# Kernel tuning notes

Hardware: AMD Instinct MI355X
Metric: run time of the kernel (lower is better)

The kernel has to match this reference:

```python
import jax, jax.numpy as jnp
import numpy as np

B, S, DIM = 4, 4096, 1024
H, DK, DV = 8, 64, 64
SEG = 512
EXP = 4
LN_EPS = 1e-5


def setup_inputs() -> dict:
    key = jax.random.key(0)
    ks = jax.random.split(key, 10)
    w = lambda i, shape: (jax.random.normal(ks[i], shape, jnp.float32) * 0.02)
    return {
        "x": jax.random.normal(ks[0], (B, S, DIM), jnp.float32),
        "Wq": w(1, (DIM, H * DK)),
        "Wk": w(2, (DIM, H * DK)),
        "Wv": w(3, (DIM, H * DV)),
        "Wo": w(4, (H * DV, DIM)),
        "betas": jax.random.normal(ks[5], (1, H, 1, DV), jnp.float32),
        "W1": w(6, (DIM, EXP * DIM)),
        "b1": jnp.zeros((EXP * DIM,), jnp.float32),
        "W2": w(7, (EXP * DIM, DIM)),
        "b2": jnp.zeros((DIM,), jnp.float32),
        "gamma": jnp.ones((DIM,), jnp.float32),
        "beta": jnp.zeros((DIM,), jnp.float32),
    }


def _compressive_memory(x, Wq, Wk, Wv, Wo, betas):
    b, s, _ = x.shape
    nseg = s // SEG
    # NOTE: original code does proj(x).unsqueeze(1).view(B, H, S, dk), i.e. a
    # pure reshape of (B, S*H*dk) -> (B, H, S, dk). We replicate it faithfully.
    qf = (x @ Wq).reshape(b, H, s, DK)
    kf = (x @ Wk).reshape(b, H, s, DK)
    vf = (x @ Wv).reshape(b, H, s, DV)
    # segment axis leading for scan: (nseg, B, H, SEG, d)
    seg_split = lambda t, d: t.reshape(b, H, nseg, SEG, d).transpose(2, 0, 1, 3, 4)
    qs, ks_, vs = seg_split(qf, DK), seg_split(kf, DK), seg_split(vf, DV)

    mem0 = jnp.zeros((b, H, DK, DV), jnp.float32)
    z0 = jnp.ones((b, H, DK, 1), jnp.float32) / DK
    causal_mask = jnp.tril(jnp.ones((SEG, SEG), bool))
    sig_b = jax.nn.sigmoid(betas)  # (1,H,1,DV)
    scale = 1.0 / (DK ** 0.5)

    def step(carry, seg):
        mem, z = carry
        q, k, v = seg  # (B,H,SEG,dk/dv)
        sigma_q = jax.nn.elu(q) + 1.0
        # memory retrieval
        att_mem = (sigma_q @ mem) / (sigma_q @ z)  # (B,H,SEG,DV)
        # local dot-product attention (causal)
        scores = jnp.einsum('bhik,bhjk->bhij', q, k) * scale
        scores = jnp.where(causal_mask, scores, -jnp.inf)
        att_dot = jax.nn.softmax(scores, axis=-1) @ v
        # linear memory update
        sigma_k = jax.nn.elu(k) + 1.0
        mem = mem + jnp.einsum('bhsk,bhsv->bhkv', sigma_k, v)
        z = z + sigma_k.sum(axis=-2, keepdims=True).transpose(0, 1, 3, 2)
        att = sig_b * att_mem + (1.0 - sig_b) * att_dot  # (B,H,SEG,DV)
        return (mem, z), att

    _, outs = jax.lax.scan(step, (mem0, z0), (qs, ks_, vs))
    # (nseg,B,H,SEG,DV) -> (B, nseg, SEG, H, DV) -> (B, S, H*DV)
    att = outs.transpose(1, 0, 3, 2, 4).reshape(b, s, H * DV)
    return att @ Wo


def reference(x, Wq, Wk, Wv, Wo, betas, W1, b1, W2, b2, gamma, beta):
    x_ = _compressive_memory(x, Wq, Wk, Wv, Wo, betas)
    # MLP: Linear -> ReLU -> Linear (dropout is identity at p=0.0)
    h = jax.nn.relu(x_ @ W1 + b1)
    x_ = h @ W2 + b2
    # residual + LayerNorm
    y = x_ + x
    mu = y.mean(axis=-1, keepdims=True)
    var = y.var(axis=-1, keepdims=True)
    return (y - mu) * jax.lax.rsqrt(var + LN_EPS) * gamma + beta
```

## Files before the change

kernel.cpp:

```cpp
#include <hip/hip_runtime.h>


typedef __attribute__((ext_vector_type(8))) short    short8;
typedef __attribute__((ext_vector_type(4))) float    f32x4;
typedef __attribute__((ext_vector_type(8))) unsigned short u16x8;
typedef __attribute__((ext_vector_type(4))) unsigned short u16x4;

#define B_    4
#define S_    4096
#define H_    8
#define SEG_  512
#define NSEG_ 8
#define QKVN  1536

__device__ __forceinline__ float bf2f(unsigned short u) {
  union { unsigned int i; float f; } x; x.i = ((unsigned int)u) << 16; return x.f;
}
__device__ __forceinline__ unsigned short f2bf(float f) {
  union { float f; unsigned int i; } x; x.f = f;
  unsigned int r = x.i + 0x7FFFu + ((x.i >> 16) & 1u);
  return (unsigned short)(r >> 16);
}
__device__ __forceinline__ float elu1(float x) { return x > 0.f ? x + 1.f : __expf(x); }

__device__ __forceinline__ void async_load16(const unsigned short* g, unsigned short* l) {
  __builtin_amdgcn_global_load_lds((const __attribute__((address_space(1))) void*)g,
                                   (__attribute__((address_space(3))) void*)l, 16, 0, 0);
}
__device__ __forceinline__ void wg_barrier() {
  asm volatile("" ::: "memory");
  __builtin_amdgcn_s_barrier();
  asm volatile("" ::: "memory");
}
__device__ __forceinline__ void vm_wait4() { asm volatile("s_waitcnt vmcnt(4)" ::: "memory"); }
__device__ __forceinline__ void vm_wait0() { asm volatile("s_waitcnt vmcnt(0)" ::: "memory"); }

__device__ __forceinline__ size_t qkv_addr(int b, int h, int seg, int i_seg, int d, int blk) {
  int r = h * 512 + seg * 64 + (i_seg >> 3);
  int c = ((i_seg & 7) << 6) + d;
  return ((size_t)b * S_ + r) * QKVN + blk + c;
}

__global__ void dtype_probe(const unsigned short* __restrict__ g, int* __restrict__ flag) {
  __shared__ int cnt;
  if (threadIdx.x == 0) cnt = 0;
  __syncthreads();
  int c = 0;
  for (int i = threadIdx.x; i < 1024; i += 256) c += (g[i] == 0x3F80u) ? 1 : 0;
  atomicAdd(&cnt, c);
  __syncthreads();
  if (threadIdx.x == 0) flag[0] = (cnt <= 768) ? 1 : 0;
}

__global__ void convert_small(const void* __restrict__ in, unsigned short* __restrict__ out,
                              int n, const int* __restrict__ flagp) {
  int i = blockIdx.x * 256 + threadIdx.x;
  if (i >= n) return;
  out[i] = (*flagp) ? f2bf(((const float*)in)[i]) : ((const unsigned short*)in)[i];
}

__global__ __launch_bounds__(256)
void convert_x(const void* __restrict__ in, unsigned short* __restrict__ out,
               int n8, const int* __restrict__ flagp) {
  int i = blockIdx.x * 256 + threadIdx.x;
  if (i >= n8) return;
  if (*flagp) {
    const f32x4* p = (const f32x4*)in;
    f32x4 a = p[(size_t)i * 2], b = p[(size_t)i * 2 + 1];
    u16x8 o;
    for (int j = 0; j < 4; j++) { o[j] = f2bf(a[j]); o[j + 4] = f2bf(b[j]); }
    *(u16x8*)(out + (size_t)i * 8) = o;
  } else {
    *(u16x8*)(out + (size_t)i * 8) = ((const u16x8*)in)[i];
  }
}

__global__ void transpose_any(const void* __restrict__ in, unsigned short* __restrict__ out,
                              int K, int N, const int* __restrict__ flagp) {
  __shared__ unsigned short tile[32][33];
  const int isf = *flagp;
  int n0 = blockIdx.x * 32, k0 = blockIdx.y * 32;
  int tx = threadIdx.x, ty = threadIdx.y;
  for (int j = 0; j < 4; j++) {
    size_t idx = (size_t)(k0 + ty + j * 8) * N + n0 + tx;
    tile[ty + j * 8][tx] = isf ? f2bf(((const float*)in)[idx]) : ((const unsigned short*)in)[idx];
  }
  __syncthreads();
  for (int j = 0; j < 4; j++)
    out[(size_t)(n0 + ty + j * 8) * K + k0 + tx] = tile[tx][ty + j * 8];
}

template <int HAS_BIAS, int RELU>
__global__ __launch_bounds__(512, 2)
void gemm256(const unsigned short* __restrict__ A,
             const unsigned short* __restrict__ Bt,
             const unsigned short* __restrict__ bias,
             unsigned short* __restrict__ C,
             int M, int N, int K) {
  __shared__ unsigned short smem[2][2][2][8192];
  const int tid = threadIdx.x;
  const int lane = tid & 63;
  const int w = tid >> 6;
  const int wr = w >> 2, wc = w & 3;
  const int l15 = lane & 15, quad = lane >> 4, l7 = lane & 7;

  const int nbx = N >> 8;
  const int nwg = (M >> 8) * nbx;
  const int orig = blockIdx.x;
  const int swz = (orig & 7) * (nwg >> 3) + (orig >> 3);
  const int m0 = (swz / nbx) << 8, n0 = (swz % nbx) << 8;

  const int srh = lane >> 3;
  const int sc = ((lane & 7) ^ srh) << 3;

  unsigned short* const A0p = &smem[0][0][0][0];
  unsigned short* const B0p = &smem[0][1][0][0];
  unsigned short* const A1p = &smem[1][0][0][0];
  unsigned short* const B1p = &smem[1][1][0][0];

  auto stA = [&](unsigned short* dst, int h, int kt) {
#pragma unroll
    for (int i2 = 0; i2 < 2; i2++) {
      const int seg = (i2 << 3) + w;
      const int r = (seg << 3) + srh;
      const int g = ((r >> 6) << 7) + (h << 6) + (r & 63);
      async_load16(A + (size_t)(m0 + g) * K + (kt << 6) + sc,
                   dst + (h << 13) + (seg << 9));
    }
  };
  auto stB = [&](unsigned short* dst, int h, int kt) {
#pragma unroll
    for (int i2 = 0; i2 < 2; i2++) {
      const int seg = (i2 << 3) + w;
      const int r = (seg << 3) + srh;
      const int g = ((r >> 5) << 6) + (h << 5) + (r & 31);
      async_load16(Bt + (size_t)(n0 + g) * K + (kt << 6) + sc,
                   dst + (h << 13) + (seg << 9));
    }
  };

  f32x4 acc[2][2][4][2] = {};
  short8 af[4][2], bfr[2][2];
  const int arow = (wr << 6) + l15;
  const int brow = (wc << 5) + l15;
  const int c0 = (quad ^ l7) << 3;
  const int c1 = ((4 + quad) ^ l7) << 3;

#define RD_A(BASE, MH) \
  { _Pragma("unroll") for (int mi = 0; mi < 4; mi++) { \
      const unsigned short* p_ = (BASE) + ((MH) << 13) + ((arow + mi * 16) << 6); \
      af[mi][0] = *(const short8*)(p_ + c0); \
      af[mi][1] = *(const short8*)(p_ + c1); } }
#define RD_B(BASE, NH) \
  { _Pragma("unroll") for (int ni = 0; ni < 2; ni++) { \
      const unsigned short* p_ = (BASE) + ((NH) << 13) + ((brow + ni * 16) << 6); \
      bfr[ni][0] = *(const short8*)(p_ + c0); \
      bfr[ni][1] = *(const short8*)(p_ + c1); } }
#define MFMA_Q(MH, NH) \
  { __builtin_amdgcn_s_setprio(1); \
    _Pragma("unroll") for (int mi = 0; mi < 4; mi++) \
    _Pragma("unroll") for (int ni = 0; ni < 2; ni++) { \
      acc[MH][NH][mi][ni] = __builtin_amdgcn_mfma_f32_16x16x32_bf16(af[mi][0], bfr[ni][0], acc[MH][NH][mi][ni], 0, 0, 0); \
      acc[MH][NH][mi][ni] = __builtin_amdgcn_mfma_f32_16x16x32_bf16(af[mi][1], bfr[ni][1], acc[MH][NH][mi][ni], 0, 0, 0); } \
    __builtin_amdgcn_s_setprio(0); }

  stA(A0p, 0, 0); stB(B0p, 1, 0); stA(A0p, 1, 0); stB(B0p, 0, 0);
  stA(A1p, 0, 1); stB(B1p, 1, 1);
  vm_wait4();
  wg_barrier();

  const int NI = K >> 7;
  for (int i = 0; i < NI; i++) {
    const int kt = i << 1;
    const bool nx = (i + 1 < NI);
    RD_A(A0p, 0) RD_B(B0p, 0)
    stA(A1p, 1, kt + 1);
    wg_barrier(); MFMA_Q(0, 0) wg_barrier();
    RD_B(B0p, 1)
    stB(B1p, 0, kt + 1);
    wg_barrier(); MFMA_Q(0, 1) wg_barrier();
    RD_A(A0p, 1)
    if (nx) stA(A0p, 0, kt + 2);
    wg_barrier(); MFMA_Q(1, 1) wg_barrier();
    RD_B(B0p, 0)
    if (nx) stB(B0p, 1, kt + 2);
    wg_barrier(); MFMA_Q(1, 0)
    if (nx) vm_wait4(); else vm_wait0();
    wg_barrier();
    RD_A(A1p, 0) RD_B(B1p, 0)
    if (nx) stA(A0p, 1, kt + 2);
    wg_barrier(); MFMA_Q(0, 0) wg_barrier();
    RD_B(B1p, 1)
    if (nx) stB(B0p, 0, kt + 2);
    wg_barrier(); MFMA_Q(0, 1) wg_barrier();
    RD_A(A1p, 1)
    if (nx) stA(A1p, 0, kt + 3);
    wg_barrier(); MFMA_Q(1, 1) wg_barrier();
    RD_B(B1p, 0)
    if (nx) stB(B1p, 1, kt + 3);
    wg_barrier(); MFMA_Q(1, 0)
    if (nx) vm_wait4(); else vm_wait0();
    wg_barrier();
  }
#undef RD_A
#undef RD_B
#undef MFMA_Q

#pragma unroll
  for (int mh = 0; mh < 2; mh++)
#pragma unroll
    for (int nh = 0; nh < 2; nh++)
#pragma unroll
      for (int ni = 0; ni < 2; ni++) {
        const int col = n0 + (wc << 6) + (nh << 5) + (ni << 4) + l15;
        const float bv = HAS_BIAS ? bf2f(bias[col]) : 0.f;
#pragma unroll
        for (int mi = 0; mi < 4; mi++) {
          const int rowb = m0 + (wr << 7) + (mh << 6) + (mi << 4) + (quad << 2);
#pragma unroll
          for (int r = 0; r < 4; r++) {
            float v = acc[mh][nh][mi][ni][r] + bv;
            if (RELU) v = v > 0.f ? v : 0.f;
            C[(size_t)(rowb + r) * N + col] = f2bf(v);
          }
        }
      }
}

template <int HAS_BIAS, int RELU, int RAWA>
__global__ __launch_bounds__(256, 4)
void gemm_bt(const void* __restrict__ A, size_t aoff,
             const unsigned short* __restrict__ Bt,
             const unsigned short* __restrict__ bias,
             unsigned short* __restrict__ C, int M, int N, int K,
             const int* __restrict__ flagp) {
  __shared__ unsigned short la[128 * 32];
  __shared__ unsigned short lb[128 * 32];
  const int isf = RAWA ? flagp[0] : 0;
  const int tid  = threadIdx.x;
  const int lane = tid & 63;
  const int w    = tid >> 6;
  const int wr   = w >> 1, wc = w & 1;
  const int m0 = blockIdx.y * 128, n0 = blockIdx.x * 128;
  const int l15 = lane & 15, quad = lane >> 4;
  const int lr = lane >> 2, l4 = lane & 3;
  f32x4 acc[4][4] = {};

  const int r0 = tid >> 2, kc0 = (tid & 3) * 8;
  const int r1 = r0 + 64;

  for (int k0 = 0; k0 < K; k0 += 32) {
    u16x8 a0v, a1v;
    if (RAWA && isf) {
      const float* Af = (const float*)A;
      size_t ia0 = aoff + (size_t)(m0 + r0) * K + k0 + kc0;
      size_t ia1 = aoff + (size_t)(m0 + r1) * K + k0 + kc0;
      f32x4 p0 = *(const f32x4*)(Af + ia0), p1 = *(const f32x4*)(Af + ia0 + 4);
      f32x4 p2 = *(const f32x4*)(Af + ia1), p3 = *(const f32x4*)(Af + ia1 + 4);
      for (int j = 0; j < 4; j++) {
        a0v[j] = f2bf(p0[j]); a0v[j + 4] = f2bf(p1[j]);
        a1v[j] = f2bf(p2[j]); a1v[j + 4] = f2bf(p3[j]);
      }
    }
    __syncthreads();
    if (!(RAWA && isf)) {
      const unsigned short* Au = (const unsigned short*)A + aoff;
      for (int i = 0; i < 2; i++) {
        int row = w * 32 + i * 16 + lr;
        async_load16(Au + (size_t)(m0 + row) * K + k0 + l4 * 8, la + (w * 32 + i * 16) * 32);
      }
    }
    for (int i = 0; i < 2; i++) {
      int row = w * 32 + i * 16 + lr;
      async_load16(Bt + (size_t)(n0 + row) * K + k0 + l4 * 8, lb + (w * 32 + i * 16) * 32);
    }
    if (RAWA && isf) {
      *(u16x8*)(la + r0 * 32 + kc0) = a0v;
      *(u16x8*)(la + r1 * 32 + kc0) = a1v;
    }
    __builtin_amdgcn_s_waitcnt(0x0F70);
    __syncthreads();
    short8 fa[4], fb[4];
    for (int mi = 0; mi < 4; mi++)
      fa[mi] = *(const short8*)(la + (wr * 64 + mi * 16 + l15) * 32 + quad * 8);
    for (int ni = 0; ni < 4; ni++)
      fb[ni] = *(const short8*)(lb + (wc * 64 + ni * 16 + l15) * 32 + quad * 8);
    for (int mi = 0; mi < 4; mi++)
      for (int ni = 0; ni < 4; ni++)
        acc[mi][ni] = __builtin_amdgcn_mfma_f32_16x16x32_bf16(fa[mi], fb[ni], acc[mi][ni], 0, 0, 0);
  }
  for (int ni = 0; ni < 4; ni++) {
    int col = n0 + wc * 64 + ni * 16 + l15;
    float bv = HAS_BIAS ? bf2f(bias[col]) : 0.f;
    for (int mi = 0; mi < 4; mi++) {
      int rowb = m0 + wr * 64 + mi * 16 + quad * 4;
      for (int r = 0; r < 4; r++) {
        float v = acc[mi][ni][r] + bv;
        if (RELU) v = v > 0.f ? v : 0.f;
        C[(size_t)(rowb + r) * N + col] = f2bf(v);
      }
    }
  }
}

__global__ __launch_bounds__(256)
void attn_stats(const unsigned short* __restrict__ qkv,
                float* __restrict__ Mseg, float* __restrict__ zseg) {
  int seg = blockIdx.x, h = blockIdx.y, b = blockIdx.z;
  __shared__ float sk[64][64];
  __shared__ float sv[64][64];
  int tid = threadIdx.x;
  int kidx = tid >> 2, vg = tid & 3;
  float acc[16] = {};
  float zacc = 0.f;
  for (int c = 0; c < 8; c++) {
    __syncthreads();
    for (int q = 0; q < 2; q++) {
      int cid = tid + q * 256;
      int row = cid >> 3, col = (cid & 7) * 8;
      int i_seg = c * 64 + row;
      u16x8 kv = *(const u16x8*)(qkv + qkv_addr(b, h, seg, i_seg, col, 512));
      u16x8 vv = *(const u16x8*)(qkv + qkv_addr(b, h, seg, i_seg, col, 1024));
      for (int j = 0; j < 8; j++) {
        sk[row][col + j] = elu1(bf2f(kv[j]));
        sv[row][col + j] = bf2f(vv[j]);
      }
    }
    __syncthreads();
    for (int i2 = 0; i2 < 64; i2++) {
      float s = sk[i2][kidx];
      if (vg == 0) zacc += s;
      for (int j = 0; j < 16; j++)
        acc[j] += s * sv[i2][vg * 16 + j];
    }
  }
  size_t ob = ((size_t)b * H_ + h) * NSEG_ + seg;
  float* mp = Mseg + ob * 4096;
  for (int j = 0; j < 16; j++)
    mp[kidx * 64 + vg * 16 + j] = acc[j];
  if (vg == 0) zseg[ob * 64 + kidx] = zacc;
}

__global__ __launch_bounds__(256)
void attn_prefix(float* __restrict__ Mseg, float* __restrict__ zseg) {
  int bh = blockIdx.x, tid = threadIdx.x;
  size_t mb = (size_t)bh * NSEG_ * 4096;
  for (int j = 0; j < 16; j++) {
    int e = tid + j * 256;
    float run = 0.f;
    for (int s = 0; s < NSEG_; s++) {
      float t = Mseg[mb + (size_t)s * 4096 + e];
      Mseg[mb + (size_t)s * 4096 + e] = run;
      run += t;
    }
  }
  if (tid < 64) {
    size_t zb = (size_t)bh * NSEG_ * 64;
    float run = 1.0f / 64.0f;
    for (int s = 0; s < NSEG_; s++) {
      float t = zseg[zb + (size_t)s * 64 + tid];
      zseg[zb + (size_t)s * 64 + tid] = run;
      run += t;
    }
  }
}

__global__ __launch_bounds__(256, 2)
void attn_core(const unsigned short* __restrict__ qkv, const unsigned short* __restrict__ betas_bf,
               const float* __restrict__ Mpre, const float* __restrict__ zpre,
               unsigned short* __restrict__ att) {
  const int t = blockIdx.x, seg = blockIdx.y;
  const int h = blockIdx.z & 7, b = blockIdx.z >> 3;
  __shared__ unsigned short q_lds[64 * 72];
  __shared__ unsigned short sq_lds[64 * 72];
  __shared__ unsigned short k_lds[64 * 72];
  __shared__ unsigned short vt_lds[64 * 72];
  __shared__ unsigned short p_lds[64 * 72];
  __shared__ unsigned short mt_lds[64 * 72];
  __shared__ float z_lds[64];
  __shared__ float den_lds[64];
  const int tid = threadIdx.x, lane = tid & 63, w = tid >> 6;
  const int l15 = lane & 15, quad = lane >> 4;
  size_t sbi = ((size_t)b * H_ + h) * NSEG_ + seg;
  const float* mp = Mpre + sbi * 4096;
  const float* zp = zpre + sbi * 64;

  for (int c = 0; c < 2; c++) {
    int idx = tid + c * 256;
    int row = idx >> 3, d0 = (idx & 7) * 8;
    u16x8 qv = *(const u16x8*)(qkv + qkv_addr(b, h, seg, t * 64 + row, d0, 0));
    u16x8 sv;
    for (int j = 0; j < 8; j++) sv[j] = f2bf(elu1(bf2f(qv[j])));
    *(u16x8*)(q_lds + row * 72 + d0) = qv;
    *(u16x8*)(sq_lds + row * 72 + d0) = sv;
    f32x4 m0 = *(const f32x4*)(mp + row * 64 + d0);
    f32x4 m1 = *(const f32x4*)(mp + row * 64 + d0 + 4);
    for (int j = 0; j < 4; j++) {
      mt_lds[(d0 + j) * 72 + row] = f2bf(m0[j]);
      mt_lds[(d0 + 4 + j) * 72 + row] = f2bf(m1[j]);
    }
  }
  if (tid < 64) z_lds[tid] = zp[tid];
  __syncthreads();
  if (tid < 64) {
    float d = 0.f;
    for (int k = 0; k < 64; k++) d += bf2f(sq_lds[tid * 72 + k]) * z_lds[k];
    den_lds[tid] = d;
  }
  f32x4 macc[4] = {};
  short8 qa0, qa1;
  {
    short8 a0 = *(const short8*)(sq_lds + (w * 16 + l15) * 72 + quad * 8);
    short8 a1 = *(const short8*)(sq_lds + (w * 16 + l15) * 72 + 32 + quad * 8);
    for (int nt = 0; nt < 4; nt++) {
      short8 b0 = *(const short8*)(mt_lds + (nt * 16 + l15) * 72 + quad * 8);
      short8 b1 = *(const short8*)(mt_lds + (nt * 16 + l15) * 72 + 32 + quad * 8);
      macc[nt] = __builtin_amdgcn_mfma_f32_16x16x32_bf16(a0, b0, macc[nt], 0, 0, 0);
      macc[nt] = __builtin_amdgcn_mfma_f32_16x16x32_bf16(a1, b1, macc[nt], 0, 0, 0);
    }
    qa0 = *(const short8*)(q_lds + (w * 16 + l15) * 72 + quad * 8);
    qa1 = *(const short8*)(q_lds + (w * 16 + l15) * 72 + 32 + quad * 8);
  }

  f32x4 oacc[4] = {};
  float lsum[4] = {0.f, 0.f, 0.f, 0.f};
  for (int kt = 0; kt <= t; kt++) {
    __syncthreads();
    for (int c = 0; c < 2; c++) {
      int idx = tid + c * 256;
      int row = idx >> 3, d0 = (idx & 7) * 8;
      u16x8 kv = *(const u16x8*)(qkv + qkv_addr(b, h, seg, kt * 64 + row, d0, 512));
      *(u16x8*)(k_lds + row * 72 + d0) = kv;
      u16x8 vv = *(const u16x8*)(qkv + qkv_addr(b, h, seg, kt * 64 + row, d0, 1024));
      for (int j = 0; j < 8; j++) vt_lds[(d0 + j) * 72 + row] = vv[j];
    }
    __syncthreads();
    float prow[4][4];
    for (int nt = 0; nt < 4; nt++) {
      short8 kb0 = *(const short8*)(k_lds + (nt * 16 + l15) * 72 + quad * 8);
      short8 kb1 = *(const short8*)(k_lds + (nt * 16 + l15) * 72 + 32 + quad * 8);
      f32x4 s = {};
      s = __builtin_amdgcn_mfma_f32_16x16x32_bf16(qa0, kb0, s, 0, 0, 0);
      s = __builtin_amdgcn_mfma_f32_16x16x32_bf16(qa1, kb1, s, 0, 0, 0);
      int jseg = kt * 64 + nt * 16 + l15;
      for (int r = 0; r < 4; r++) {
        int iseg = t * 64 + w * 16 + quad * 4 + r;
        prow[nt][r] = (jseg <= iseg) ? __expf(s[r] * 0.125f) : 0.f;
      }
    }
    for (int r = 0; r < 4; r++) {
      float rp = prow[0][r] + prow[1][r] + prow[2][r] + prow[3][r];
      rp += __shfl_xor(rp, 1); rp += __shfl_xor(rp, 2);
      rp += __shfl_xor(rp, 4); rp += __shfl_xor(rp, 8);
      lsum[r] += rp;
    }
    for (int nt = 0; nt < 4; nt++)
      for (int r = 0; r < 4; r++)
        p_lds[(w * 16 + quad * 4 + r) * 72 + nt * 16 + l15] = f2bf(prow[nt][r]);
    __syncthreads();
    short8 pa0 = *(const short8*)(p_lds + (w * 16 + l15) * 72 + quad * 8);
    short8 pa1 = *(const short8*)(p_lds + (w * 16 + l15) * 72 + 32 + quad * 8);
    for (int nt = 0; nt < 4; nt++) {
      short8 vb0 = *(const short8*)(vt_lds + (nt * 16 + l15) * 72 + quad * 8);
      short8 vb1 = *(const short8*)(vt_lds + (nt * 16 + l15) * 72 + 32 + quad * 8);
      oacc[nt] = __builtin_amdgcn_mfma_f32_16x16x32_bf16(pa0, vb0, oacc[nt], 0, 0, 0);
      oacc[nt] = __builtin_amdgcn_mfma_f32_16x16x32_bf16(pa1, vb1, oacc[nt], 0, 0, 0);
    }
  }
  __syncthreads();
  for (int nt = 0; nt < 4; nt++) {
    int v = nt * 16 + l15;
    float sb = 1.f / (1.f + __expf(-bf2f(betas_bf[h * 64 + v])));
    for (int r = 0; r < 4; r++) {
      int irow = w * 16 + quad * 4 + r;
      float am = macc[nt][r] / den_lds[irow];
      float ad = oacc[nt][r] / lsum[r];
      float o = sb * am + (1.f - sb) * ad;
      size_t orow = (size_t)b * S_ + (size_t)seg * SEG_ + t * 64 + irow;
      att[orow * 512 + h * 64 + v] = f2bf(o);
    }
  }
}

__global__ __launch_bounds__(256)
void ln_kernel(const unsigned short* __restrict__ x2, const void* __restrict__ xraw,
               const unsigned short* __restrict__ gamma_bf, const unsigned short* __restrict__ beta_bf,
               void* __restrict__ out, const int* __restrict__ flagp) {
  const int isf = *flagp;
  int row = blockIdx.x, tid = threadIdx.x;
  size_t rb = (size_t)row * 1024;
  u16x4 a = *(const u16x4*)(x2 + rb + tid * 4);
  float xv[4];
  if (isf) {
    f32x4 tv = *(const f32x4*)((const float*)xraw + rb + tid * 4);
    for (int j = 0; j < 4; j++) xv[j] = tv[j];
  } else {
    u16x4 tv = *(const u16x4*)((const unsigned short*)xraw + rb + tid * 4);
    for (int j = 0; j < 4; j++) xv[j] = bf2f(tv[j]);
  }
  float vv[4], s = 0.f, ss = 0.f;
  for (int j = 0; j < 4; j++) {
    vv[j] = bf2f(a[j]) + xv[j];
    s += vv[j]; ss += vv[j] * vv[j];
  }
  for (int off = 32; off >= 1; off >>= 1) { s += __shfl_xor(s, off); ss += __shfl_xor(ss, off); }
  __shared__ float ps[4], pss[4];
  int w = tid >> 6, lane = tid & 63;
  if (lane == 0) { ps[w] = s; pss[w] = ss; }
  __syncthreads();
  if (tid == 0) {
    float S = 0.f, SS = 0.f;
    for (int k = 0; k < 4; k++) { S += ps[k]; SS += pss[k]; }
    ps[0] = S; pss[0] = SS;
  }
  __syncthreads();
  float mean = ps[0] * (1.f / 1024.f);
  float var = pss[0] * (1.f / 1024.f) - mean * mean;
  float rs = rsqrtf(var + 1e-5f);
  u16x4 g = *(const u16x4*)(gamma_bf + tid * 4);
  u16x4 be = *(const u16x4*)(beta_bf + tid * 4);
  if (isf) {
    f32x4 o;
    for (int j = 0; j < 4; j++) o[j] = (vv[j] - mean) * rs * bf2f(g[j]) + bf2f(be[j]);
    *(f32x4*)((float*)out + rb + tid * 4) = o;
  } else {
    u16x4 o;
    for (int j = 0; j < 4; j++) o[j] = f2bf((vv[j] - mean) * rs * bf2f(g[j]) + bf2f(be[j]));
    *(u16x4*)((unsigned short*)out + rb + tid * 4) = o;
  }
}

extern "C" void kernel_launch(void* const* d_in, const int* in_sizes, int n_in,
                              void* d_out, int out_size, void* d_ws, size_t ws_size,
                              hipStream_t stream) {
  const void* x     = d_in[0];
  const void* Wq    = d_in[1];
  const void* Wk    = d_in[2];
  const void* Wv    = d_in[3];
  const void* Wo    = d_in[4];
  const void* betas = d_in[5];
  const void* W1    = d_in[6];
  const void* b1    = d_in[7];
  const void* W2    = d_in[8];
  const void* b2    = d_in[9];
  const void* gamma = d_in[10];
  const void* beta  = d_in[11];

  char* ws = (char*)d_ws;
  size_t off = 0;
  auto alloc = [&](size_t bytes) { char* p = ws + off; off += (bytes + 255) & ~(size_t)255; return p; };

  const int M = B_ * S_;
  int* flag = (int*)alloc(256);
  unsigned short* W1T = (unsigned short*)alloc((size_t)4096 * 1024 * 2);
  unsigned short* W2T = (unsigned short*)alloc((size_t)1024 * 4096 * 2);
  unsigned short* WqkvT = (unsigned short*)alloc((size_t)QKVN * 1024 * 2);
  unsigned short* WoT = (unsigned short*)alloc((size_t)1024 * 512 * 2);
  unsigned short* betas_bf = (unsigned short*)alloc(512 * 2);
  unsigned short* b1_bf    = (unsigned short*)alloc(4096 * 2);
  unsigned short* b2_bf    = (unsigned short*)alloc(1024 * 2);
  unsigned short* gamma_bf = (unsigned short*)alloc(1024 * 2);
  unsigned short* beta_bf  = (unsigned short*)alloc(1024 * 2);
  float* Mseg = (float*)alloc((size_t)B_ * H_ * NSEG_ * 4096 * 4);
  float* zseg = (float*)alloc((size_t)B_ * H_ * NSEG_ * 64 * 4);
  unsigned short* qkvb = (unsigned short*)alloc((size_t)M * QKVN * 2);
  unsigned short* x1   = qkvb;
  unsigned short* xbf  = (unsigned short*)d_out;
  unsigned short* attb = (unsigned short*)d_out;
  unsigned short* hbuf = (unsigned short*)d_out;

  if (off > ws_size) return;

  dtype_probe<<<1, 256, 0, stream>>>((const unsigned short*)gamma, flag);
  convert_small<<<2, 256, 0, stream>>>(betas, betas_bf, 512, flag);
  convert_small<<<16, 256, 0, stream>>>(b1, b1_bf, 4096, flag);
  convert_small<<<4, 256, 0, stream>>>(b2, b2_bf, 1024, flag);
  convert_small<<<4, 256, 0, stream>>>(gamma, gamma_bf, 1024, flag);
  convert_small<<<4, 256, 0, stream>>>(beta, beta_bf, 1024, flag);

  dim3 tb(32, 8);
  transpose_any<<<dim3(16, 32), tb, 0, stream>>>(Wq, WqkvT, 1024, 512, flag);
  transpose_any<<<dim3(16, 32), tb, 0, stream>>>(Wk, WqkvT + (size_t)512 * 1024, 1024, 512, flag);
  transpose_any<<<dim3(16, 32), tb, 0, stream>>>(Wv, WqkvT + (size_t)1024 * 1024, 1024, 512, flag);
  transpose_any<<<dim3(32, 16), tb, 0, stream>>>(Wo, WoT, 512, 1024, flag);
  transpose_any<<<dim3(128, 32), tb, 0, stream>>>(W1, W1T, 1024, 4096, flag);
  transpose_any<<<dim3(32, 128), tb, 0, stream>>>(W2, W2T, 4096, 1024, flag);

  convert_x<<<dim3((M * 1024 / 8 + 255) / 256), 256, 0, stream>>>(x, xbf, M * 1024 / 8, flag);

  gemm256<0, 0><<<dim3(384), 512, 0, stream>>>(xbf, WqkvT, nullptr, qkvb, M, QKVN, 1024);

  attn_stats<<<dim3(NSEG_, H_, B_), 256, 0, stream>>>(qkvb, Mseg, zseg);
  attn_prefix<<<dim3(B_ * H_), 256, 0, stream>>>(Mseg, zseg);
  attn_core<<<dim3(8, NSEG_, H_ * B_), 256, 0, stream>>>(qkvb, betas_bf, Mseg, zseg, attb);

  gemm256<0, 0><<<dim3(256), 512, 0, stream>>>(attb, WoT, nullptr, x1, M, 1024, 512);

  for (int c = 0; c < 2; c++) {
    unsigned short* x1c = x1 + (size_t)c * 8192 * 1024;
    gemm256<1, 1><<<dim3(512), 512, 0, stream>>>(x1c, W1T, b1_bf, hbuf, 8192, 4096, 1024);
    gemm_bt<1, 0, 0><<<dim3(8, 64), 256, 0, stream>>>(hbuf, 0, W2T, b2_bf, x1c, 8192, 1024, 4096, flag);
  }

  ln_kernel<<<dim3(M), 256, 0, stream>>>(x1, x, gamma_bf, beta_bf, d_out, flag);
}
```

Before: 776.3 us.

## Run MLP as whole-batch GEMMs with 256-tile kernel for W2 projection

The second MLP GEMM now uses the larger 256x256-tile gemm256 kernel instead of the 128-tile gemm_bt kernel, which is removed. When the workspace can hold the full 16384x4096 hidden activation, both MLP GEMMs run once over all rows instead of in two halves. This gives larger grids and fewer launches. The cost is a larger workspace buffer, and the W2 GEMM with 256 tiles has few blocks (256 or 128) relative to the CU count.

After: 695.3 us. 1.12x faster.

```diff
diff --git a/kernel.cpp b/kernel.cpp
--- a/kernel.cpp
+++ b/kernel.cpp
@@ -227,82 +227,6 @@
       }
 }
 
-template <int HAS_BIAS, int RELU, int RAWA>
-__global__ __launch_bounds__(256, 4)
-void gemm_bt(const void* __restrict__ A, size_t aoff,
-             const unsigned short* __restrict__ Bt,
-             const unsigned short* __restrict__ bias,
-             unsigned short* __restrict__ C, int M, int N, int K,
-             const int* __restrict__ flagp) {
-  __shared__ unsigned short la[128 * 32];
-  __shared__ unsigned short lb[128 * 32];
-  const int isf = RAWA ? flagp[0] : 0;
-  const int tid  = threadIdx.x;
-  const int lane = tid & 63;
-  const int w    = tid >> 6;
-  const int wr   = w >> 1, wc = w & 1;
-  const int m0 = blockIdx.y * 128, n0 = blockIdx.x * 128;
-  const int l15 = lane & 15, quad = lane >> 4;
-  const int lr = lane >> 2, l4 = lane & 3;
-  f32x4 acc[4][4] = {};
-
-  const int r0 = tid >> 2, kc0 = (tid & 3) * 8;
-  const int r1 = r0 + 64;
-
-  for (int k0 = 0; k0 < K; k0 += 32) {
-    u16x8 a0v, a1v;
-    if (RAWA && isf) {
-      const float* Af = (const float*)A;
-      size_t ia0 = aoff + (size_t)(m0 + r0) * K + k0 + kc0;
-      size_t ia1 = aoff + (size_t)(m0 + r1) * K + k0 + kc0;
-      f32x4 p0 = *(const f32x4*)(Af + ia0), p1 = *(const f32x4*)(Af + ia0 + 4);
-      f32x4 p2 = *(const f32x4*)(Af + ia1), p3 = *(const f32x4*)(Af + ia1 + 4);
-      for (int j = 0; j < 4; j++) {
-        a0v[j] = f2bf(p0[j]); a0v[j + 4] = f2bf(p1[j]);
-        a1v[j] = f2bf(p2[j]); a1v[j + 4] = f2bf(p3[j]);
-      }
-    }
-    __syncthreads();
-    if (!(RAWA && isf)) {
-      const unsigned short* Au = (const unsigned short*)A + aoff;
-      for (int i = 0; i < 2; i++) {
-        int row = w * 32 + i * 16 + lr;
-        async_load16(Au + (size_t)(m0 + row) * K + k0 + l4 * 8, la + (w * 32 + i * 16) * 32);
-      }
-    }
-    for (int i = 0; i < 2; i++) {
-      int row = w * 32 + i * 16 + lr;
-      async_load16(Bt + (size_t)(n0 + row) * K + k0 + l4 * 8, lb + (w * 32 + i * 16) * 32);
-    }
-    if (RAWA && isf) {
-      *(u16x8*)(la + r0 * 32 + kc0) = a0v;
-      *(u16x8*)(la + r1 * 32 + kc0) = a1v;
-    }
-    __builtin_amdgcn_s_waitcnt(0x0F70);
-    __syncthreads();
-    short8 fa[4], fb[4];
-    for (int mi = 0; mi < 4; mi++)
-      fa[mi] = *(const short8*)(la + (wr * 64 + mi * 16 + l15) * 32 + quad * 8);
-    for (int ni = 0; ni < 4; ni++)
-      fb[ni] = *(const short8*)(lb + (wc * 64 + ni * 16 + l15) * 32 + quad * 8);
-    for (int mi = 0; mi < 4; mi++)
-      for (int ni = 0; ni < 4; ni++)
-        acc[mi][ni] = __builtin_amdgcn_mfma_f32_16x16x32_bf16(fa[mi], fb[ni], acc[mi][ni], 0, 0, 0);
-  }
-  for (int ni = 0; ni < 4; ni++) {
-    int col = n0 + wc * 64 + ni * 16 + l15;
-    float bv = HAS_BIAS ? bf2f(bias[col]) : 0.f;
-    for (int mi = 0; mi < 4; mi++) {
-      int rowb = m0 + wr * 64 + mi * 16 + quad * 4;
-      for (int r = 0; r < 4; r++) {
-        float v = acc[mi][ni][r] + bv;
-        if (RELU) v = v > 0.f ? v : 0.f;
-        C[(size_t)(rowb + r) * N + col] = f2bf(v);
-      }
-    }
-  }
-}
-
 __global__ __launch_bounds__(256)
 void attn_stats(const unsigned short* __restrict__ qkv,
                 float* __restrict__ Mseg, float* __restrict__ zseg) {
@@ -567,9 +491,14 @@
   unsigned short* x1   = qkvb;
   unsigned short* xbf  = (unsigned short*)d_out;
   unsigned short* attb = (unsigned short*)d_out;
-  unsigned short* hbuf = (unsigned short*)d_out;
+  unsigned short* hsml = (unsigned short*)d_out;
 
   if (off > ws_size) return;
+
+  size_t off_save = off;
+  unsigned short* hbig = (unsigned short*)alloc((size_t)M * 4096 * 2);
+  const bool bigws = (off <= ws_size);
+  if (!bigws) off = off_save;
 
   dtype_probe<<<1, 256, 0, stream>>>((const unsigned short*)gamma, flag);
   convert_small<<<2, 256, 0, stream>>>(betas, betas_bf, 512, flag);
@@ -596,10 +525,15 @@
 
   gemm256<0, 0><<<dim3(256), 512, 0, stream>>>(attb, WoT, nullptr, x1, M, 1024, 512);
 
-  for (int c = 0; c < 2; c++) {
-    unsigned short* x1c = x1 + (size_t)c * 8192 * 1024;
-    gemm256<1, 1><<<dim3(512), 512, 0, stream>>>(x1c, W1T, b1_bf, hbuf, 8192, 4096, 1024);
-    gemm_bt<1, 0, 0><<<dim3(8, 64), 256, 0, stream>>>(hbuf, 0, W2T, b2_bf, x1c, 8192, 1024, 4096, flag);
+  if (bigws) {
+    gemm256<1, 1><<<dim3(1024), 512, 0, stream>>>(x1, W1T, b1_bf, hbig, M, 4096, 1024);
+    gemm256<1, 0><<<dim3(256), 512, 0, stream>>>(hbig, W2T, b2_bf, x1, M, 1024, 4096);
+  } else {
+    for (int c = 0; c < 2; c++) {
+      unsigned short* x1c = x1 + (size_t)c * 8192 * 1024;
+      gemm256<1, 1><<<dim3(512), 512, 0, stream>>>(x1c, W1T, b1_bf, hsml, 8192, 4096, 1024);
+      gemm256<1, 0><<<dim3(128), 512, 0, stream>>>(hsml, W2T, b2_bf, x1c, 8192, 1024, 4096);
+    }
   }
 
   ln_kernel<<<dim3(M), 256, 0, stream>>>(x1, x, gamma_bf, beta_bf, d_out, flag);
```
